# Kernel tuning notes

Hardware: AMD Instinct MI355X
Metric: run time of the kernel (lower is better)

The kernel has to match this reference:

```python
import jax, jax.numpy as jnp
import numpy as np

BATCH = 50000
MULS = (256, 256, 128)   # multiplicities of 0e, 1o, 2e
DIMS = (1, 3, 5)         # irrep dims (2l+1)
TOTAL = sum(m * d for m, d in zip(MULS, DIMS))  # 1664
# path_normalization='element', gradient_normalization='path' with one
# instruction per output irrep => path_weight = sqrt(1/mul_in), weight_std = 1
PATH_W = tuple(np.float32(1.0 / np.sqrt(m)) for m in MULS)


def setup_inputs() -> dict:
    key = jax.random.key(0)
    k = jax.random.split(key, 4)
    x = jax.random.normal(k[0], (BATCH, TOTAL), dtype=jnp.float32)
    w0 = jax.random.normal(k[1], (MULS[0], MULS[0]), dtype=jnp.float32)
    w1 = jax.random.normal(k[2], (MULS[1], MULS[1]), dtype=jnp.float32)
    w2 = jax.random.normal(k[3], (MULS[2], MULS[2]), dtype=jnp.float32)
    return {"x": x, "w0": w0, "w1": w1, "w2": w2}


def reference(x, w0, w1, w2):
    # For each irrep block: reshape to [B, mul, ir_dim], contract mul with the
    # per-instruction weight ('uw,ui->wi' batched), scale by path_weight,
    # and place into the corresponding output slice (here: concatenate).
    ws = (w0, w1, w2)
    out_blocks = []
    off = 0
    for w, mul, dim, pw in zip(ws, MULS, DIMS, PATH_W):
        seg = x[:, off:off + mul * dim].reshape(-1, mul, dim)  # [B, u, i]
        y = pw * jnp.einsum('uw,bui->bwi', w, seg)             # [B, w, i]
        out_blocks.append(y.reshape(x.shape[0], mul * dim))
        off += mul * dim
    return jnp.concatenate(out_blocks, axis=-1)  # [B, 1664]
```

## Files before the change

kernel.cpp:

```cpp
#include <hip/hip_runtime.h>


typedef __attribute__((ext_vector_type(8))) short short8;
typedef __attribute__((ext_vector_type(4))) float f32x4;

#define NBATCH 50000
#define NTOTAL 1664

__device__ __forceinline__ unsigned short f2bf(float f) {
    union { float f; unsigned u; } v; v.f = f;
    unsigned r = v.u + 0x7fffu + ((v.u >> 16) & 1u);
    return (unsigned short)(r >> 16);
}

__global__ void prep_kernel(const float* __restrict__ w0,
                            const float* __restrict__ w1,
                            const float* __restrict__ w2,
                            unsigned short* __restrict__ ws) {
    int e = blockIdx.x * blockDim.x + threadIdx.x;
    const float* W; int N, base;
    if (e < 65536)       { W = w0; N = 256; base = 0; }
    else if (e < 131072) { W = w1; N = 256; base = 65536;  e -= 65536; }
    else if (e < 147456) { W = w2; N = 128; base = 131072; e -= 131072; }
    else return;
    int j = e & 7;
    int lane = (e >> 3) & 63;
    int qt = e >> 9;
    int NT = N >> 4;
    int t = qt % NT;
    int q = qt / NT;
    int u = q * 32 + ((lane >> 4) << 3) + j;
    int w = t * 16 + (lane & 15);
    ws[base + e] = f2bf(W[u * N + w]);
}

template<int D, int K, int NT, int NTW, int OFF>
__device__ __forceinline__ void run_block(const float* __restrict__ x,
                                          float* __restrict__ out,
                                          const short8* __restrict__ bsw,
                                          float pw,
                                          char* __restrict__ sm) {
    constexpr int COLS   = K * D;
    constexpr int C4     = COLS / 4;
    constexpr int RB     = COLS * 2;
    constexpr int ROUNDS = (16 * C4) / 256;

    const int tid  = threadIdx.x;
    const int lane = tid & 63;
    const int wave = tid >> 6;
    const int b0   = blockIdx.x << 4;

#pragma unroll
    for (int rr = 0; rr < ROUNDS; ++rr) {
        int c    = rr * 256 + tid;
        int row  = c / C4;
        int col4 = c - row * C4;
        float4 v = *((const float4*)(x + (size_t)(b0 + row) * NTOTAL + OFF)
                     + col4);
        unsigned long long pk =
              (unsigned long long)f2bf(v.x)
            | ((unsigned long long)f2bf(v.y) << 16)
            | ((unsigned long long)f2bf(v.z) << 32)
            | ((unsigned long long)f2bf(v.w) << 48);
        *(unsigned long long*)(sm + row * RB + ((col4 * 8) ^ ((row & 7) << 4)))
            = pk;
    }
    __syncthreads();

    const int bcol = lane & 15;
    const int quad = lane >> 4;
    const char* lrow = sm + bcol * RB;
    const int sw = (bcol & 7) << 4;

    f32x4 acc[NTW][D];
#pragma unroll
    for (int tt = 0; tt < NTW; ++tt)
#pragma unroll
        for (int i = 0; i < D; ++i)
            acc[tt][i] = (f32x4){0.f, 0.f, 0.f, 0.f};

#pragma unroll
    for (int q = 0; q < K / 32; ++q) {
        const int cb = (q * 32 + quad * 8) * D * 2;
        short8 raw[D];
#pragma unroll
        for (int m = 0; m < D; ++m)
            raw[m] = *(const short8*)(lrow + ((cb + m * 16) ^ sw));

        short8 af[D];
#pragma unroll
        for (int i = 0; i < D; ++i)
#pragma unroll
            for (int j = 0; j < 8; ++j) {
                const int e = j * D + i;
                af[i][j] = raw[e >> 3][e & 7];
            }

#pragma unroll
        for (int tt = 0; tt < NTW; ++tt) {
            const int t = wave * NTW + tt;
            short8 bf = bsw[(q * NT + t) * 64 + lane];
#pragma unroll
            for (int i = 0; i < D; ++i)
                acc[tt][i] = __builtin_amdgcn_mfma_f32_16x16x32_bf16(
                    af[i], bf, acc[tt][i], 0, 0, 0);
        }
    }

#pragma unroll
    for (int tt = 0; tt < NTW; ++tt) {
        const int wcol = (wave * NTW + tt) * 16 + bcol;
#pragma unroll
        for (int r = 0; r < 4; ++r) {
            float* op = out + (size_t)(b0 + quad * 4 + r) * NTOTAL + OFF
                        + wcol * D;
#pragma unroll
            for (int i = 0; i < D; ++i)
                op[i] = acc[tt][i][r] * pw;
        }
    }
}

__global__ __launch_bounds__(256, 4)
void linear_kernel(const float* __restrict__ x, float* __restrict__ out,
                   const unsigned short* __restrict__ ws) {
    __shared__ __attribute__((aligned(16))) char sm[24576];
    const short8* bs0 = (const short8*)(ws);
    const short8* bs1 = (const short8*)(ws + 65536);
    const short8* bs2 = (const short8*)(ws + 131072);
    if (blockIdx.y == 0)
        run_block<1, 256, 16, 4, 0>(x, out, bs0, 0.0625f, sm);
    else if (blockIdx.y == 1)
        run_block<3, 256, 16, 4, 256>(x, out, bs1, 0.0625f, sm);
    else
        run_block<5, 128, 8, 2, 1024>(x, out, bs2, 0.08838834764831845f, sm);
}

extern "C" void kernel_launch(void* const* d_in, const int* in_sizes, int n_in,
                              void* d_out, int out_size, void* d_ws,
                              size_t ws_size, hipStream_t stream) {
    const float* x  = (const float*)d_in[0];
    const float* w0 = (const float*)d_in[1];
    const float* w1 = (const float*)d_in[2];
    const float* w2 = (const float*)d_in[3];
    unsigned short* ws = (unsigned short*)d_ws;

    prep_kernel<<<dim3(576), 256, 0, stream>>>(w0, w1, w2, ws);

    dim3 grid(NBATCH / 16, 3);
    linear_kernel<<<grid, 256, 0, stream>>>(x, (float*)d_out, ws);
}
```

Before: 564.3 us.

## Process several batch tiles per block with register prefetch of next tile

Each block now walks five consecutive 16-row batch tiles instead of one, cutting the grid size by five. While the MFMA loop runs on the current tile, the next tile's x data is loaded into registers, then converted and written to LDS after a barrier. The aim is to hide global load latency behind compute and amortise block launch overhead. In exchange it adds register pressure (launch bounds relaxed from 4 to 3 blocks per CU), two extra barriers per tile, and fewer blocks to spread across the GPU.

```diff
diff --git a/kernel.cpp b/kernel.cpp
--- a/kernel.cpp
+++ b/kernel.cpp
@@ -34,7 +34,7 @@
     ws[base + e] = f2bf(W[u * N + w]);
 }
 
-template<int D, int K, int NT, int NTW, int OFF>
+template<int D, int K, int NT, int NTW, int OFF, int TP>
 __device__ __forceinline__ void run_block(const float* __restrict__ x,
                                           float* __restrict__ out,
                                           const short8* __restrict__ bsw,
@@ -48,23 +48,38 @@
     const int tid  = threadIdx.x;
     const int lane = tid & 63;
     const int wave = tid >> 6;
-    const int b0   = blockIdx.x << 4;
+    const int tile0 = blockIdx.x * TP;
 
+    float4 pf[ROUNDS];
+    auto load_pf = [&](int tile) {
 #pragma unroll
-    for (int rr = 0; rr < ROUNDS; ++rr) {
-        int c    = rr * 256 + tid;
-        int row  = c / C4;
-        int col4 = c - row * C4;
-        float4 v = *((const float4*)(x + (size_t)(b0 + row) * NTOTAL + OFF)
-                     + col4);
-        unsigned long long pk =
-              (unsigned long long)f2bf(v.x)
-            | ((unsigned long long)f2bf(v.y) << 16)
-            | ((unsigned long long)f2bf(v.z) << 32)
-            | ((unsigned long long)f2bf(v.w) << 48);
-        *(unsigned long long*)(sm + row * RB + ((col4 * 8) ^ ((row & 7) << 4)))
-            = pk;
-    }
+        for (int rr = 0; rr < ROUNDS; ++rr) {
+            int c    = rr * 256 + tid;
+            int row  = c / C4;
+            int col4 = c - row * C4;
+            pf[rr] = *((const float4*)
+                       (x + (size_t)(tile * 16 + row) * NTOTAL + OFF) + col4);
+        }
+    };
+    auto write_lds = [&]() {
+#pragma unroll
+        for (int rr = 0; rr < ROUNDS; ++rr) {
+            int c    = rr * 256 + tid;
+            int row  = c / C4;
+            int col4 = c - row * C4;
+            float4 v = pf[rr];
+            unsigned long long pk =
+                  (unsigned long long)f2bf(v.x)
+                | ((unsigned long long)f2bf(v.y) << 16)
+                | ((unsigned long long)f2bf(v.z) << 32)
+                | ((unsigned long long)f2bf(v.w) << 48);
+            *(unsigned long long*)(sm + row * RB
+                                   + ((col4 * 8) ^ ((row & 7) << 4))) = pk;
+        }
+    };
+
+    load_pf(tile0);
+    write_lds();
     __syncthreads();
 
     const int bcol = lane & 15;
@@ -72,56 +87,67 @@
     const char* lrow = sm + bcol * RB;
     const int sw = (bcol & 7) << 4;
 
-    f32x4 acc[NTW][D];
+    for (int t = 0; t < TP; ++t) {
+        if (t + 1 < TP) load_pf(tile0 + t + 1);
+
+        f32x4 acc[NTW][D];
 #pragma unroll
-    for (int tt = 0; tt < NTW; ++tt)
+        for (int tt = 0; tt < NTW; ++tt)
 #pragma unroll
-        for (int i = 0; i < D; ++i)
-            acc[tt][i] = (f32x4){0.f, 0.f, 0.f, 0.f};
+            for (int i = 0; i < D; ++i)
+                acc[tt][i] = (f32x4){0.f, 0.f, 0.f, 0.f};
 
 #pragma unroll
-    for (int q = 0; q < K / 32; ++q) {
-        const int cb = (q * 32 + quad * 8) * D * 2;
-        short8 raw[D];
+        for (int q = 0; q < K / 32; ++q) {
+            const int cb = (q * 32 + quad * 8) * D * 2;
+            short8 raw[D];
 #pragma unroll
-        for (int m = 0; m < D; ++m)
-            raw[m] = *(const short8*)(lrow + ((cb + m * 16) ^ sw));
+            for (int m = 0; m < D; ++m)
+                raw[m] = *(const short8*)(lrow + ((cb + m * 16) ^ sw));
 
-        short8 af[D];
+            short8 af[D];
 #pragma unroll
-        for (int i = 0; i < D; ++i)
+            for (int i = 0; i < D; ++i)
 #pragma unroll
-            for (int j = 0; j < 8; ++j) {
-                const int e = j * D + i;
-                af[i][j] = raw[e >> 3][e & 7];
-            }
+                for (int j = 0; j < 8; ++j) {
+                    const int e = j * D + i;
+                    af[i][j] = raw[e >> 3][e & 7];
+                }
 
 #pragma unroll
+            for (int tt = 0; tt < NTW; ++tt) {
+                const int tw = wave * NTW + tt;
+                short8 bf = bsw[(q * NT + tw) * 64 + lane];
+#pragma unroll
+                for (int i = 0; i < D; ++i)
+                    acc[tt][i] = __builtin_amdgcn_mfma_f32_16x16x32_bf16(
+                        af[i], bf, acc[tt][i], 0, 0, 0);
+            }
+        }
+
+        const int b0 = (tile0 + t) << 4;
+#pragma unroll
         for (int tt = 0; tt < NTW; ++tt) {
-            const int t = wave * NTW + tt;
-            short8 bf = bsw[(q * NT + t) * 64 + lane];
+            const int wcol = (wave * NTW + tt) * 16 + bcol;
 #pragma unroll
-            for (int i = 0; i < D; ++i)
-                acc[tt][i] = __builtin_amdgcn_mfma_f32_16x16x32_bf16(
-                    af[i], bf, acc[tt][i], 0, 0, 0);
+            for (int r = 0; r < 4; ++r) {
+                float* op = out + (size_t)(b0 + quad * 4 + r) * NTOTAL + OFF
+                            + wcol * D;
+#pragma unroll
+                for (int i = 0; i < D; ++i)
+                    op[i] = acc[tt][i][r] * pw;
+            }
         }
-    }
 
-#pragma unroll
-    for (int tt = 0; tt < NTW; ++tt) {
-        const int wcol = (wave * NTW + tt) * 16 + bcol;
-#pragma unroll
-        for (int r = 0; r < 4; ++r) {
-            float* op = out + (size_t)(b0 + quad * 4 + r) * NTOTAL + OFF
-                        + wcol * D;
-#pragma unroll
-            for (int i = 0; i < D; ++i)
-                op[i] = acc[tt][i][r] * pw;
+        __syncthreads();
+        if (t + 1 < TP) {
+            write_lds();
+            __syncthreads();
         }
     }
 }
 
-__global__ __launch_bounds__(256, 4)
+__global__ __launch_bounds__(256, 3)
 void linear_kernel(const float* __restrict__ x, float* __restrict__ out,
                    const unsigned short* __restrict__ ws) {
     __shared__ __attribute__((aligned(16))) char sm[24576];
@@ -129,11 +155,12 @@
     const short8* bs1 = (const short8*)(ws + 65536);
     const short8* bs2 = (const short8*)(ws + 131072);
     if (blockIdx.y == 0)
-        run_block<1, 256, 16, 4, 0>(x, out, bs0, 0.0625f, sm);
+        run_block<1, 256, 16, 4, 0, 5>(x, out, bs0, 0.0625f, sm);
     else if (blockIdx.y == 1)
-        run_block<3, 256, 16, 4, 256>(x, out, bs1, 0.0625f, sm);
+        run_block<3, 256, 16, 4, 256, 5>(x, out, bs1, 0.0625f, sm);
     else
-        run_block<5, 128, 8, 2, 1024>(x, out, bs2, 0.08838834764831845f, sm);
+        run_block<5, 128, 8, 2, 1024, 5>(x, out, bs2,
+                                         0.08838834764831845f, sm);
 }
 
 extern "C" void kernel_launch(void* const* d_in, const int* in_sizes, int n_in,
@@ -147,6 +174,6 @@
 
     prep_kernel<<<dim3(576), 256, 0, stream>>>(w0, w1, w2, ws);
 
-    dim3 grid(NBATCH / 16, 3);
+    dim3 grid(NBATCH / 16 / 5, 3);
     linear_kernel<<<grid, 256, 0, stream>>>(x, (float*)d_out, ws);
 }
```

Measured after the change: 735.7 us. +30.4%, slower.
